# Performance work log

Hardware: AMD Instinct MI355X
Metric: run time of the kernel (lower is better)

Reference implementation:

```python
import jax, jax.numpy as jnp
import numpy as np

B, N, C, H = 8, 2048, 512, 8
D = C // H                      # head dim = 64
Q_LENGTHS = [1024 + 128 * i for i in range(B)]  # ragged: 1024..1920, sum below
TQ = sum(Q_LENGTHS)             # 11776 total queries


def setup_inputs() -> dict:
    key = jax.random.key(0)
    ks = jax.random.split(key, 5)
    w = 0.02  # init scale for weights
    return {
        "x": jax.random.normal(ks[0], (B, N, C), jnp.float32),
        "q": jax.random.normal(ks[1], (TQ, C), jnp.float32),
        "Wq": jax.random.normal(ks[2], (C, C), jnp.float32) * w,
        "Wkv": jax.random.normal(ks[3], (2 * C, C), jnp.float32) * w,
        "Wproj": jax.random.normal(ks[4], (C, C), jnp.float32) * w,
        "bproj": jnp.zeros((C,), jnp.float32),
        "q_lengths": jnp.array(Q_LENGTHS, jnp.int32),
        "max_q_len": max(Q_LENGTHS),
    }


def reference(x, q, Wq, Wkv, Wproj, bproj, q_lengths, max_q_len):
    # Eval path of Attention.forward: batched_sparse_attention(q, k, v, q_lengths, scale)
    # == varlen cross-attention: queries of batch b attend over all N kv tokens of batch b.
    Tq = q.shape[0]
    scale = D ** -0.5

    qh = (q @ Wq.T).reshape(Tq, H, D)                 # [Tq, H, D]
    kv = (x @ Wkv.T).reshape(B, N, 2, H, D)
    k = kv[:, :, 0]                                   # [B, N, H, D]
    v = kv[:, :, 1]                                   # [B, N, H, D]

    # ragged -> padded per-batch layout
    csum = jnp.cumsum(q_lengths)                      # [B]
    offs = jnp.concatenate([jnp.zeros((1,), csum.dtype), csum])
    tok = jnp.arange(Tq)
    q_batch = (tok[:, None] >= csum[None, :]).sum(-1)  # [Tq] batch id per query
    q_pos = tok - offs[q_batch]                        # [Tq] position within batch

    qpad = jnp.zeros((B, max_q_len, H, D), qh.dtype).at[q_batch, q_pos].set(qh)

    scores = jnp.einsum('blhd,bnhd->bhln', qpad, k) * scale  # [B, H, L, N]
    attn = jax.nn.softmax(scores, axis=-1)                   # all N keys valid
    out = jnp.einsum('bhln,bnhd->blhd', attn, v)             # [B, L, H, D]

    out = out[q_batch, q_pos].reshape(Tq, C)           # gather ragged rows back
    return out @ Wproj.T + bproj
```

## Files before the change

kernel.cpp:

```cpp
#include <hip/hip_runtime.h>
#include <hip/hip_bf16.h>
#include <math.h>

constexpr int Cc = 512;
constexpr int Hh = 8;
constexpr int Dd = 64;
constexpr int Nn = 2048;
constexpr int Bb = 8;
constexpr int GK = 512;

typedef __attribute__((ext_vector_type(8))) short short8;
typedef __attribute__((ext_vector_type(4))) float f32x4;
typedef __attribute__((ext_vector_type(4))) unsigned int u32x4;
typedef __attribute__((ext_vector_type(2))) unsigned int u32x2;

#define C2SCALE 0.1803368801f

static __device__ __forceinline__ ushort f2bf(float v) {
  __hip_bfloat16 h = __float2bfloat16(v);
  return *reinterpret_cast<ushort*>(&h);
}
static __device__ __forceinline__ float bf2f(ushort u) {
  __hip_bfloat16 h = *reinterpret_cast<__hip_bfloat16*>(&u);
  return __bfloat162float(h);
}
static __device__ __forceinline__ unsigned int pk2(float f0, float f1) {
  return (unsigned int)f2bf(f0) | ((unsigned int)f2bf(f1) << 16);
}

__global__ __launch_bounds__(256) void mfma_proj_kernel(
    const ushort* __restrict__ Ah, const ushort* __restrict__ Al,
    const float* __restrict__ Bf, const float* __restrict__ bias,
    float* __restrict__ Cf, int Nc)
{
  __shared__ ushort lAh[128 * 32];
  __shared__ ushort lBh[128 * 32];
  __shared__ ushort lAl[128 * 32];
  __shared__ ushort lBl[128 * 32];

  const int tid = threadIdx.x;
  const int w = tid >> 6, lane = tid & 63;
  const int c = lane & 15, g = lane >> 4;
  const int wr = (w >> 1) * 64, wc = (w & 1) * 64;
  const int m0 = blockIdx.y * 128, n0 = blockIdx.x * 128;
  const int sr = tid >> 2;
  const int sk = (tid & 3) * 8;

  short8 rAh[2], rAl[2], rBh[2], rBl[2];

  auto ldf32 = [&](const float* F, size_t idx, short8& h, short8& l) {
    const float4 f0 = *(const float4*)(F + idx);
    const float4 f1 = *(const float4*)(F + idx + 4);
    const float vv[8] = {f0.x, f0.y, f0.z, f0.w, f1.x, f1.y, f1.z, f1.w};
#pragma unroll
    for (int j = 0; j < 8; ++j) {
      const ushort hb = f2bf(vv[j]);
      ((ushort*)&h)[j] = hb;
      ((ushort*)&l)[j] = f2bf(vv[j] - bf2f(hb));
    }
  };

  auto loadAB = [&](int k0) {
#pragma unroll
    for (int hf = 0; hf < 2; ++hf) {
      const size_t ia = (size_t)(m0 + sr + hf * 64) * GK + k0 + sk;
      const size_t ib = (size_t)(n0 + sr + hf * 64) * GK + k0 + sk;
      rAh[hf] = *(const short8*)(Ah + ia);
      rAl[hf] = *(const short8*)(Al + ia);
      ldf32(Bf, ib, rBh[hf], rBl[hf]);
    }
  };

  f32x4 acc[4][4] = {};
  loadAB(0);

  for (int k0 = 0; k0 < GK; k0 += 32) {
    __syncthreads();
    *(short8*)&lAh[sr * 32 + sk]        = rAh[0];
    *(short8*)&lAh[(sr + 64) * 32 + sk] = rAh[1];
    *(short8*)&lBh[sr * 32 + sk]        = rBh[0];
    *(short8*)&lBh[(sr + 64) * 32 + sk] = rBh[1];
    *(short8*)&lAl[sr * 32 + sk]        = rAl[0];
    *(short8*)&lAl[(sr + 64) * 32 + sk] = rAl[1];
    *(short8*)&lBl[sr * 32 + sk]        = rBl[0];
    *(short8*)&lBl[(sr + 64) * 32 + sk] = rBl[1];
    __syncthreads();
    if (k0 + 32 < GK) loadAB(k0 + 32);

    short8 ah[4], al[4], bh[4], bl[4];
#pragma unroll
    for (int i = 0; i < 4; ++i) {
      const int ar = (wr + i * 16 + c) * 32 + g * 8;
      const int br = (wc + i * 16 + c) * 32 + g * 8;
      ah[i] = *(const short8*)&lAh[ar];
      bh[i] = *(const short8*)&lBh[br];
      al[i] = *(const short8*)&lAl[ar];
      bl[i] = *(const short8*)&lBl[br];
    }
#pragma unroll
    for (int mi = 0; mi < 4; ++mi)
#pragma unroll
      for (int nj = 0; nj < 4; ++nj) {
        acc[mi][nj] = __builtin_amdgcn_mfma_f32_16x16x32_bf16(ah[mi], bl[nj], acc[mi][nj], 0,0,0);
        acc[mi][nj] = __builtin_amdgcn_mfma_f32_16x16x32_bf16(al[mi], bh[nj], acc[mi][nj], 0,0,0);
        acc[mi][nj] = __builtin_amdgcn_mfma_f32_16x16x32_bf16(ah[mi], bh[nj], acc[mi][nj], 0,0,0);
      }
  }

#pragma unroll
  for (int mi = 0; mi < 4; ++mi)
#pragma unroll
    for (int r = 0; r < 4; ++r) {
      const size_t rb = (size_t)(m0 + wr + mi * 16 + g * 4 + r) * Nc;
#pragma unroll
      for (int nj = 0; nj < 4; ++nj) {
        const int col = n0 + wc + nj * 16 + c;
        Cf[rb + col] = acc[mi][nj][r] + bias[col];
      }
    }
}

__global__ __launch_bounds__(256, 2) void proj_qkv_kernel(
    const float* __restrict__ qin, const float* __restrict__ Wq,
    const float* __restrict__ x, const float* __restrict__ Wkv,
    ushort* __restrict__ qhi, ushort* __restrict__ kbf,
    ushort* __restrict__ vtb, int TQ, int BN)
{
  __shared__ ushort smem[128 * 136];

  const int tid = threadIdx.x;
  const int w = tid >> 6, lane = tid & 63;
  const int c = lane & 15, g = lane >> 4;
  const int wr = (w >> 1) * 64, wc = (w & 1) * 64;
  const int sr = tid >> 2, sk = (tid & 3) * 8;
  const int NQB = (TQ / 128) * (Cc / 128);
  const int bid = blockIdx.x;

  auto cvt8 = [&](const float* F, size_t idx) -> short8 {
    const float4 f0 = *(const float4*)(F + idx);
    const float4 f1 = *(const float4*)(F + idx + 4);
    const float vv[8] = {f0.x, f0.y, f0.z, f0.w, f1.x, f1.y, f1.z, f1.w};
    short8 h;
#pragma unroll
    for (int j = 0; j < 8; ++j) ((ushort*)&h)[j] = f2bf(vv[j]);
    return h;
  };

  if (bid < NQB) {
    const int m0 = (bid >> 2) * 128;
    const int n0 = (bid & 3) * 128;
    ushort* lA = smem;
    ushort* lB = smem + 128 * 32;

    short8 rA[2], rB[2];
    auto loadQ = [&](int k0) {
#pragma unroll
      for (int hf = 0; hf < 2; ++hf) {
        rA[hf] = cvt8(qin, (size_t)(m0 + sr + hf * 64) * GK + k0 + sk);
        rB[hf] = cvt8(Wq,  (size_t)(n0 + sr + hf * 64) * GK + k0 + sk);
      }
    };

    f32x4 acc[4][4] = {};
    loadQ(0);
    for (int k0 = 0; k0 < GK; k0 += 32) {
      __syncthreads();
      *(short8*)&lA[sr * 32 + sk]        = rA[0];
      *(short8*)&lA[(sr + 64) * 32 + sk] = rA[1];
      *(short8*)&lB[sr * 32 + sk]        = rB[0];
      *(short8*)&lB[(sr + 64) * 32 + sk] = rB[1];
      __syncthreads();
      if (k0 + 32 < GK) loadQ(k0 + 32);

      short8 a[4], bb[4];
#pragma unroll
      for (int i = 0; i < 4; ++i) {
        a[i]  = *(const short8*)&lA[(wr + i * 16 + c) * 32 + g * 8];
        bb[i] = *(const short8*)&lB[(wc + i * 16 + c) * 32 + g * 8];
      }
#pragma unroll
      for (int mi = 0; mi < 4; ++mi)
#pragma unroll
        for (int nj = 0; nj < 4; ++nj)
          acc[mi][nj] = __builtin_amdgcn_mfma_f32_16x16x32_bf16(a[mi], bb[nj], acc[mi][nj], 0,0,0);
    }
#pragma unroll
    for (int mi = 0; mi < 4; ++mi)
#pragma unroll
      for (int r = 0; r < 4; ++r) {
        const size_t rb = (size_t)(m0 + wr + mi * 16 + g * 4 + r) * Cc;
#pragma unroll
        for (int nj = 0; nj < 4; ++nj)
          qhi[rb + n0 + wc + nj * 16 + c] = f2bf(acc[mi][nj][r] * C2SCALE);
      }
  } else {
    const int b2 = bid - NQB;
    const int n0 = (b2 & 3) * 128;
    const int m0 = (b2 >> 2) * 128;
    ushort* lA   = smem;
    ushort* lBk  = smem + 128 * 32;
    ushort* lBv  = smem + 2 * 128 * 32;
    ushort* tbuf = smem;

    short8 rA[2], rBk[2], rBv[2];
    auto loadAll = [&](int k0) {
#pragma unroll
      for (int hf = 0; hf < 2; ++hf) {
        rA[hf]  = cvt8(x,   (size_t)(m0 + sr + hf * 64) * GK + k0 + sk);
        rBk[hf] = cvt8(Wkv, (size_t)(n0 + sr + hf * 64) * GK + k0 + sk);
        rBv[hf] = cvt8(Wkv, (size_t)(512 + n0 + sr + hf * 64) * GK + k0 + sk);
      }
    };

    f32x4 ak[4][4] = {};
    f32x4 av[4][4] = {};
    loadAll(0);

    for (int k0 = 0; k0 < GK; k0 += 32) {
      __syncthreads();
      *(short8*)&lA[sr * 32 + sk]         = rA[0];
      *(short8*)&lA[(sr + 64) * 32 + sk]  = rA[1];
      *(short8*)&lBk[sr * 32 + sk]        = rBk[0];
      *(short8*)&lBk[(sr + 64) * 32 + sk] = rBk[1];
      *(short8*)&lBv[sr * 32 + sk]        = rBv[0];
      *(short8*)&lBv[(sr + 64) * 32 + sk] = rBv[1];
      __syncthreads();
      if (k0 + 32 < GK) loadAll(k0 + 32);

      short8 a[4], bk[4], bv[4];
#pragma unroll
      for (int i = 0; i < 4; ++i) {
        const int ar = (wr + i * 16 + c) * 32 + g * 8;
        const int br = (wc + i * 16 + c) * 32 + g * 8;
        a[i]  = *(const short8*)&lA[ar];
        bk[i] = *(const short8*)&lBk[br];
        bv[i] = *(const short8*)&lBv[br];
      }
#pragma unroll
      for (int mi = 0; mi < 4; ++mi)
#pragma unroll
        for (int nj = 0; nj < 4; ++nj) {
          ak[mi][nj] = __builtin_amdgcn_mfma_f32_16x16x32_bf16(a[mi], bk[nj], ak[mi][nj], 0,0,0);
          av[mi][nj] = __builtin_amdgcn_mfma_f32_16x16x32_bf16(a[mi], bv[nj], av[mi][nj], 0,0,0);
        }
    }

#pragma unroll
    for (int mi = 0; mi < 4; ++mi)
#pragma unroll
      for (int r = 0; r < 4; ++r) {
        const size_t rb = (size_t)(m0 + wr + mi * 16 + g * 4 + r) * Cc;
#pragma unroll
        for (int nj = 0; nj < 4; ++nj)
          kbf[rb + n0 + wc + nj * 16 + c] = f2bf(ak[mi][nj][r]);
      }

    __syncthreads();
#pragma unroll
    for (int mi = 0; mi < 4; ++mi)
#pragma unroll
      for (int r = 0; r < 4; ++r) {
        const int tl = wr + mi * 16 + g * 4 + r;
#pragma unroll
        for (int nj = 0; nj < 4; ++nj)
          tbuf[(wc + nj * 16 + c) * 136 + tl] = f2bf(av[mi][nj][r]);
      }
    __syncthreads();
#pragma unroll
    for (int it = 0; it < 8; ++it) {
      const int idx = tid + it * 256;
      const int row = idx >> 4;
      const int c8 = (idx & 15) * 8;
      *(short8*)&vtb[(size_t)(n0 + row) * BN + m0 + c8] =
          *(const short8*)&tbuf[row * 136 + c8];
    }
  }
}

__global__ __launch_bounds__(256, 4) void attn_mfma14_kernel(
    const ushort* __restrict__ qhi,
    const ushort* __restrict__ kbf,
    const ushort* __restrict__ vtb,
    ushort* __restrict__ ohi,
    ushort* __restrict__ olo)
{
  constexpr int QOFF[8] = {0, 1024, 2176, 3456, 4864, 6400, 8064, 9856};

  const int lin = blockIdx.x;
  const int b  = lin & 7;
  const int h  = (lin >> 3) & 7;
  const int qt = lin >> 6;

  const int Lb  = 1024 + 128 * b;
  const int off = QOFF[b];
  if (qt * 128 >= Lb) return;

  constexpr int KP = 72;
  constexpr int NC = Nn / 64;
  __shared__ ushort Ks[64 * KP];
  __shared__ ushort Vs[64 * KP];

  const int tid = threadIdx.x;
  const int lane = tid & 63;
  const int w = tid >> 6;
  const int c = lane & 15;
  const int g = (lane >> 4) & 3;

  short8 qf[2][2];
  int qrow[2];
#pragma unroll
  for (int t = 0; t < 2; ++t) {
    qrow[t] = off + qt * 128 + w * 32 + t * 16 + c;
    const size_t base = (size_t)qrow[t] * Cc + h * Dd + g * 8;
    qf[t][0] = *(const short8*)(qhi + base);
    qf[t][1] = *(const short8*)(qhi + base + 32);
  }

  float l_part[2] = {0.f, 0.f};
  f32x4 accO4[2][4] = {};

  const size_t kbase = (size_t)b * Nn * Cc + h * Dd;
  const size_t vbase = (size_t)h * Dd * (Bb * Nn) + (size_t)b * Nn;

  for (int ch = 0; ch < NC; ++ch) {
    __syncthreads();
#pragma unroll
    for (int it = 0; it < 2; ++it) {
      const int i = tid + it * 256;
      const int row = i >> 3, c8 = (i & 7) * 8;
      *(short8*)&Ks[row * KP + c8] =
          *(const short8*)&kbf[kbase + (size_t)(ch * 64 + row) * Cc + c8];
    }
#pragma unroll
    for (int it = 0; it < 2; ++it) {
      const int i = tid + it * 256;
      const int row = i >> 3, c8 = (i & 7) * 8;
      const int kb1 = (c8 & ~31) | (((c8 >> 3) & 3) << 2);
      const size_t gb = vbase + (size_t)row * (Bb * Nn) + ch * 64;
      const u32x2 vlo = *(const u32x2*)&vtb[gb + kb1];
      const u32x2 vhi = *(const u32x2*)&vtb[gb + kb1 + 16];
      u32x4 vv;
      vv[0] = vlo[0]; vv[1] = vlo[1];
      vv[2] = vhi[0]; vv[3] = vhi[1];
      *(short8*)&Vs[row * KP + c8] = __builtin_bit_cast(short8, vv);
    }
    __syncthreads();

    f32x4 accT4[2][4] = {};
    __builtin_amdgcn_s_setprio(1);
#pragma unroll
    for (int ks2 = 0; ks2 < 2; ++ks2) {
#pragma unroll
      for (int kb = 0; kb < 4; ++kb) {
        const short8 kf = *(const short8*)
            &Ks[(kb * 16 + c) * KP + ks2 * 32 + g * 8];
        accT4[0][kb] = __builtin_amdgcn_mfma_f32_16x16x32_bf16(kf, qf[0][ks2], accT4[0][kb], 0,0,0);
        accT4[1][kb] = __builtin_amdgcn_mfma_f32_16x16x32_bf16(kf, qf[1][ks2], accT4[1][kb], 0,0,0);
      }
    }
    __builtin_amdgcn_s_setprio(0);

    unsigned int up[2][4][2];
#pragma unroll
    for (int t = 0; t < 2; ++t)
#pragma unroll
      for (int kb = 0; kb < 4; ++kb) {
        const float p0 = __builtin_amdgcn_exp2f(accT4[t][kb][0]);
        const float p1 = __builtin_amdgcn_exp2f(accT4[t][kb][1]);
        const float p2 = __builtin_amdgcn_exp2f(accT4[t][kb][2]);
        const float p3 = __builtin_amdgcn_exp2f(accT4[t][kb][3]);
        l_part[t] += (p0 + p1) + (p2 + p3);
        up[t][kb][0] = pk2(p0, p1);
        up[t][kb][1] = pk2(p2, p3);
      }

#pragma unroll
    for (int ks2 = 0; ks2 < 2; ++ks2) {
      short8 pa[2];
#pragma unroll
      for (int t = 0; t < 2; ++t) {
        u32x4 wv;
        wv.x = up[t][2 * ks2][0];
        wv.y = up[t][2 * ks2][1];
        wv.z = up[t][2 * ks2 + 1][0];
        wv.w = up[t][2 * ks2 + 1][1];
        pa[t] = __builtin_bit_cast(short8, wv);
      }
      __builtin_amdgcn_s_setprio(1);
#pragma unroll
      for (int db = 0; db < 4; ++db) {
        const short8 vf = *(const short8*)
            &Vs[(db * 16 + c) * KP + ks2 * 32 + g * 8];
        accO4[0][db] = __builtin_amdgcn_mfma_f32_16x16x32_bf16(vf, pa[0], accO4[0][db], 0,0,0);
        accO4[1][db] = __builtin_amdgcn_mfma_f32_16x16x32_bf16(vf, pa[1], accO4[1][db], 0,0,0);
      }
      __builtin_amdgcn_s_setprio(0);
    }
  }

#pragma unroll
  for (int t = 0; t < 2; ++t) {
    float l = l_part[t];
    l += __shfl_xor(l, 16);
    l += __shfl_xor(l, 32);
    const float inv = 1.f / l;
    const size_t rb = (size_t)qrow[t] * Cc + h * Dd;
#pragma unroll
    for (int db = 0; db < 4; ++db) {
      const int d0 = db * 16 + g * 4;
      ushort4 uh, ul;
#pragma unroll
      for (int e = 0; e < 4; ++e) {
        const float o = accO4[t][db][e] * inv;
        const ushort hb = f2bf(o);
        ((ushort*)&uh)[e] = hb;
        ((ushort*)&ul)[e] = f2bf(o - bf2f(hb));
      }
      *(ushort4*)&ohi[rb + d0] = uh;
      *(ushort4*)&olo[rb + d0] = ul;
    }
  }
}

extern "C" void kernel_launch(void* const* d_in, const int* in_sizes, int n_in,
                              void* d_out, int out_size, void* d_ws, size_t ws_size,
                              hipStream_t stream)
{
  const float* x     = (const float*)d_in[0];
  const float* q     = (const float*)d_in[1];
  const float* Wq    = (const float*)d_in[2];
  const float* Wkv   = (const float*)d_in[3];
  const float* Wproj = (const float*)d_in[4];
  const float* bproj = (const float*)d_in[5];

  const int TQ = in_sizes[1] / Cc;
  const int BN = in_sizes[0] / Cc;

  const size_t szQ = (size_t)TQ * Cc * 2;
  const size_t szX = (size_t)BN * Cc * 2;

  char* p = (char*)d_ws;
  ushort* q_hi  = (ushort*)p;  p += szQ;
  ushort* k_bf  = (ushort*)p;  p += szX;
  ushort* v_t   = (ushort*)p;  p += szX;
  ushort* at_hi = (ushort*)p;  p += szQ;
  ushort* at_lo = (ushort*)p;

  const int nqb = (TQ / 128) * (Cc / 128);
  const int nkvb = (BN / 128) * (Cc / 128);
  proj_qkv_kernel<<<dim3(nqb + nkvb), 256, 0, stream>>>(
      q, Wq, x, Wkv, q_hi, k_bf, v_t, TQ, BN);
  attn_mfma14_kernel<<<dim3(64 * 15), 256, 0, stream>>>(
      q_hi, k_bf, v_t, at_hi, at_lo);
  mfma_proj_kernel<<<dim3(Cc/128, TQ/128), 256, 0, stream>>>(
      at_hi, at_lo, Wproj, bproj, (float*)d_out, Cc);
}
```

Before: 160.3 us.

## Double-buffer K/V tiles in attention kernel with register prefetch

The attention kernel now keeps two LDS buffers for K and V. The next chunk is loaded from global memory into registers before the current chunk's MFMA work and written to the other buffer afterwards. This overlaps global load latency with compute and cuts the per-chunk barriers from two to one. It costs twice the LDS and extra registers, which may lower occupancy at the 4-blocks-per-CU launch bound.

After: 161.0 us. No clear change (+0.5%).

```diff
diff --git a/kernel.cpp b/kernel.cpp
--- a/kernel.cpp
+++ b/kernel.cpp
@@ -277,7 +277,7 @@
   }
 }
 
-__global__ __launch_bounds__(256, 4) void attn_mfma14_kernel(
+__global__ __launch_bounds__(256, 4) void attn_mfma16_kernel(
     const ushort* __restrict__ qhi,
     const ushort* __restrict__ kbf,
     const ushort* __restrict__ vtb,
@@ -297,8 +297,8 @@
 
   constexpr int KP = 72;
   constexpr int NC = Nn / 64;
-  __shared__ ushort Ks[64 * KP];
-  __shared__ ushort Vs[64 * KP];
+  __shared__ ushort Ks[2][64 * KP];
+  __shared__ ushort Vs[2][64 * KP];
 
   const int tid = threadIdx.x;
   const int lane = tid & 63;
@@ -322,29 +322,49 @@
   const size_t kbase = (size_t)b * Nn * Cc + h * Dd;
   const size_t vbase = (size_t)h * Dd * (Bb * Nn) + (size_t)b * Nn;
 
-  for (int ch = 0; ch < NC; ++ch) {
-    __syncthreads();
+  const int srK = tid >> 3, c8K = (tid & 7) * 8;
+  const int srV = tid >> 3, c8V = (tid & 7) * 8;
+  const int kb1 = (c8V & ~31) | (((c8V >> 3) & 3) << 2);
+  short8 krg[2], vrg[2];
+
+  auto loadKV = [&](int ch) {
 #pragma unroll
     for (int it = 0; it < 2; ++it) {
-      const int i = tid + it * 256;
-      const int row = i >> 3, c8 = (i & 7) * 8;
-      *(short8*)&Ks[row * KP + c8] =
-          *(const short8*)&kbf[kbase + (size_t)(ch * 64 + row) * Cc + c8];
+      const int row = srK + it * 32;
+      krg[it] = *(const short8*)&kbf[kbase + (size_t)(ch * 64 + row) * Cc + c8K];
     }
 #pragma unroll
     for (int it = 0; it < 2; ++it) {
-      const int i = tid + it * 256;
-      const int row = i >> 3, c8 = (i & 7) * 8;
-      const int kb1 = (c8 & ~31) | (((c8 >> 3) & 3) << 2);
+      const int row = srV + it * 32;
       const size_t gb = vbase + (size_t)row * (Bb * Nn) + ch * 64;
       const u32x2 vlo = *(const u32x2*)&vtb[gb + kb1];
       const u32x2 vhi = *(const u32x2*)&vtb[gb + kb1 + 16];
       u32x4 vv;
       vv[0] = vlo[0]; vv[1] = vlo[1];
       vv[2] = vhi[0]; vv[3] = vhi[1];
-      *(short8*)&Vs[row * KP + c8] = __builtin_bit_cast(short8, vv);
-    }
-    __syncthreads();
+      vrg[it] = __builtin_bit_cast(short8, vv);
+    }
+  };
+  auto writeKV = [&](int buf) {
+#pragma unroll
+    for (int it = 0; it < 2; ++it)
+      *(short8*)&Ks[buf][(srK + it * 32) * KP + c8K] = krg[it];
+#pragma unroll
+    for (int it = 0; it < 2; ++it)
+      *(short8*)&Vs[buf][(srV + it * 32) * KP + c8V] = vrg[it];
+  };
+
+  loadKV(0);
+  writeKV(0);
+  __syncthreads();
+
+  for (int ch = 0; ch < NC; ++ch) {
+    const int cur = ch & 1;
+    const bool more = (ch + 1 < NC);
+    if (more) loadKV(ch + 1);
+
+    const ushort* Kc = &Ks[cur][0];
+    const ushort* Vc = &Vs[cur][0];
 
     f32x4 accT4[2][4] = {};
     __builtin_amdgcn_s_setprio(1);
@@ -353,7 +373,7 @@
 #pragma unroll
       for (int kb = 0; kb < 4; ++kb) {
         const short8 kf = *(const short8*)
-            &Ks[(kb * 16 + c) * KP + ks2 * 32 + g * 8];
+            &Kc[(kb * 16 + c) * KP + ks2 * 32 + g * 8];
         accT4[0][kb] = __builtin_amdgcn_mfma_f32_16x16x32_bf16(kf, qf[0][ks2], accT4[0][kb], 0,0,0);
         accT4[1][kb] = __builtin_amdgcn_mfma_f32_16x16x32_bf16(kf, qf[1][ks2], accT4[1][kb], 0,0,0);
       }
@@ -390,11 +410,16 @@
 #pragma unroll
       for (int db = 0; db < 4; ++db) {
         const short8 vf = *(const short8*)
-            &Vs[(db * 16 + c) * KP + ks2 * 32 + g * 8];
+            &Vc[(db * 16 + c) * KP + ks2 * 32 + g * 8];
         accO4[0][db] = __builtin_amdgcn_mfma_f32_16x16x32_bf16(vf, pa[0], accO4[0][db], 0,0,0);
         accO4[1][db] = __builtin_amdgcn_mfma_f32_16x16x32_bf16(vf, pa[1], accO4[1][db], 0,0,0);
       }
       __builtin_amdgcn_s_setprio(0);
+    }
+
+    if (more) {
+      writeKV(cur ^ 1);
+      __syncthreads();
     }
   }
 
@@ -450,7 +475,7 @@
   const int nkvb = (BN / 128) * (Cc / 128);
   proj_qkv_kernel<<<dim3(nqb + nkvb), 256, 0, stream>>>(
       q, Wq, x, Wkv, q_hi, k_bf, v_t, TQ, BN);
-  attn_mfma14_kernel<<<dim3(64 * 15), 256, 0, stream>>>(
+  attn_mfma16_kernel<<<dim3(64 * 15), 256, 0, stream>>>(
       q_hi, k_bf, v_t, at_hi, at_lo);
   mfma_proj_kernel<<<dim3(Cc/128, TQ/128), 256, 0, stream>>>(
       at_hi, at_lo, Wproj, bproj, (float*)d_out, Cc);
```
